# Optimization experiments

Hardware: AMD Instinct MI355X
Metric: run time of the kernel (lower is better)

## Reference

```python
import jax, jax.numpy as jnp
import numpy as np

B, L, IN_SZ, MEM_SZ = 32, 2048, 256, 256
W_SCALE = 0.05  # keep tanh/sigmoid out of saturation with random weights


def setup_inputs() -> dict:
    key = jax.random.key(0)
    ks = jax.random.split(key, 6)
    u = jax.random.normal(ks[0], (B, L, IN_SZ), dtype=jnp.float32)
    mk = lambda k, o, i: jax.random.normal(k, (o, i), dtype=jnp.float32) * W_SCALE
    return {
        "u": u,
        "W_ia": mk(ks[1], MEM_SZ, IN_SZ),
        "W_ha": mk(ks[2], MEM_SZ, MEM_SZ),
        "W_ic": mk(ks[3], MEM_SZ, IN_SZ),
        "W_hc": mk(ks[4], MEM_SZ, MEM_SZ),
        "W_io": mk(ks[5], MEM_SZ, IN_SZ),
    }


def reference(u, W_ia, W_ha, W_ic, W_hc, W_io):
    # u: [B, L, in_sz]; torch Linear: y = x @ W.T (no bias).
    b, l, _ = u.shape
    mem = W_ha.shape[0]
    # Precompute all input-side projections in 3 batched GEMMs (h-independent).
    xa = jnp.einsum('bli,mi->lbm', u, W_ia)  # [L,B,M]
    xc = jnp.einsum('bli,mi->lbm', u, W_ic)
    xo = jnp.einsum('bli,mi->lbm', u, W_io)

    def step(h, xs):
        xa_t, xc_t, xo_t = xs
        a = 1.0 + jnp.tanh(xa_t + h @ W_ha.T)
        c = jax.nn.sigmoid(xc_t + h @ W_hc.T)
        h_new = c * h + (1.0 - c) * jnp.tanh(xo_t + a * h)
        return h_new, h_new

    h0 = jnp.zeros((b, mem), dtype=u.dtype)
    _, hs = jax.lax.scan(step, h0, (xa, xc, xo))  # hs: [L,B,M]
    h_seq = jnp.transpose(hs, (1, 0, 2))  # [B,L,M]
    return h_seq, h_seq[:, -1:, :]
```

## Files before the change

### kernel.cpp

```cpp
#include <hip/hip_runtime.h>
#include <stdint.h>

#ifndef __has_builtin
#define __has_builtin(x) 0
#endif
#if __has_builtin(__builtin_amdgcn_fdot2)
#define HAVE_FDOT2 1
#else
#define HAVE_FDOT2 0
#endif

typedef float    f32x4 __attribute__((ext_vector_type(4)));
typedef _Float16 f16x2 __attribute__((ext_vector_type(2)));
typedef _Float16 f16x4 __attribute__((ext_vector_type(4)));
typedef _Float16 f16x8 __attribute__((ext_vector_type(8)));

#define NB 32
#define NL 2048
#define NM 256
#define NC 768
#define XS_SCALE 4096.0f
#define XS_INV   2.44140625e-4f

__device__ __forceinline__ float dot2f(f16x2 a, f16x2 b, float c) {
#if HAVE_FDOT2
  return __builtin_amdgcn_fdot2(a, b, c, false);
#else
  float d;
  asm("v_dot2_f32_f16 %0, %1, %2, %3" : "=v"(d) : "v"(a), "v"(b), "v"(c));
  return d;
#endif
}

__device__ __forceinline__ float tanh_fast(float x) {
  x = fminf(fmaxf(x, -30.f), 30.f);
  float e = __expf(-2.f * x);
  return (1.f - e) / (1.f + e);
}
__device__ __forceinline__ float sigmoid_fast(float x) {
  x = fminf(fmaxf(x, -30.f), 30.f);
  return 1.f / (1.f + __expf(-x));
}

__global__ __launch_bounds__(256) void proj_kernel(
    const float* __restrict__ u, const float* __restrict__ Wia,
    const float* __restrict__ Wic, const float* __restrict__ Wio,
    int16_t* __restrict__ xs)
{
  __shared__ _Float16 sAh[128][72];
  __shared__ _Float16 sAl[128][72];
  __shared__ _Float16 sBh[128][72];
  __shared__ _Float16 sBl[128][72];
  const int tid = threadIdx.x;
  const int rb = blockIdx.x, cb = blockIdx.y;
  const float* W = (cb < 2) ? Wia : (cb < 4) ? Wic : Wio;
  const int wrow0 = (cb & 1) * 128;

  const int wave = tid >> 6, lane = tid & 63;
  const int wr = (wave >> 1) * 64, wc = (wave & 1) * 64;
  const int lrow = lane & 15, lk = (lane >> 4) * 8;

  f32x4 acc[4][4] = {};

  for (int kt = 0; kt < 4; ++kt) {
#pragma unroll
    for (int i = 0; i < 8; ++i) {
      int idx = tid + 256 * i;
      int r = idx >> 4, c4 = idx & 15;
      f32x4 va = *reinterpret_cast<const f32x4*>(
          u + (size_t)(rb * 128 + r) * 256 + kt * 64 + c4 * 4);
      f16x4 hh, hl;
#pragma unroll
      for (int q = 0; q < 4; ++q) {
        _Float16 hi = (_Float16)va[q];
        hh[q] = hi;
        hl[q] = (_Float16)(va[q] - (float)hi);
      }
      *reinterpret_cast<f16x4*>(&sAh[r][c4 * 4]) = hh;
      *reinterpret_cast<f16x4*>(&sAl[r][c4 * 4]) = hl;
      f32x4 vb = *reinterpret_cast<const f32x4*>(
          W + (size_t)(wrow0 + r) * 256 + kt * 64 + c4 * 4);
      f16x4 gh, gl;
#pragma unroll
      for (int q = 0; q < 4; ++q) {
        _Float16 hi = (_Float16)vb[q];
        gh[q] = hi;
        gl[q] = (_Float16)(vb[q] - (float)hi);
      }
      *reinterpret_cast<f16x4*>(&sBh[r][c4 * 4]) = gh;
      *reinterpret_cast<f16x4*>(&sBl[r][c4 * 4]) = gl;
    }
    __syncthreads();
#pragma unroll
    for (int kk = 0; kk < 2; ++kk) {
      const int k0 = kk * 32 + lk;
      f16x8 afh[4], afl[4], bfh[4], bfl[4];
#pragma unroll
      for (int i = 0; i < 4; ++i) {
        afh[i] = *reinterpret_cast<const f16x8*>(&sAh[wr + i * 16 + lrow][k0]);
        afl[i] = *reinterpret_cast<const f16x8*>(&sAl[wr + i * 16 + lrow][k0]);
      }
#pragma unroll
      for (int j = 0; j < 4; ++j) {
        bfh[j] = *reinterpret_cast<const f16x8*>(&sBh[wc + j * 16 + lrow][k0]);
        bfl[j] = *reinterpret_cast<const f16x8*>(&sBl[wc + j * 16 + lrow][k0]);
      }
#pragma unroll
      for (int i = 0; i < 4; ++i)
#pragma unroll
        for (int j = 0; j < 4; ++j) {
          acc[i][j] = __builtin_amdgcn_mfma_f32_16x16x32_f16(afl[i], bfh[j], acc[i][j], 0, 0, 0);
          acc[i][j] = __builtin_amdgcn_mfma_f32_16x16x32_f16(afh[i], bfl[j], acc[i][j], 0, 0, 0);
          acc[i][j] = __builtin_amdgcn_mfma_f32_16x16x32_f16(afh[i], bfh[j], acc[i][j], 0, 0, 0);
        }
    }
    __syncthreads();
  }

  const size_t row0 = (size_t)rb * 128 + wr + (lane >> 4) * 4;
  const int col0 = cb * 128 + wc + (lane & 15);
#pragma unroll
  for (int i = 0; i < 4; ++i)
#pragma unroll
    for (int j = 0; j < 4; ++j)
#pragma unroll
      for (int q = 0; q < 4; ++q) {
        float v = acc[i][j][q] * XS_SCALE;
        v = fminf(fmaxf(v, -32767.f), 32767.f);
        xs[(row0 + i * 16 + q) * NC + (col0 + j * 16)] = (int16_t)__float2int_rn(v);
      }
}

__global__ __launch_bounds__(1024, 1) void rec_kernel(
    const float* __restrict__ Wha, const float* __restrict__ Whc,
    const int16_t* __restrict__ xs, float* __restrict__ out)
{
  __shared__ __align__(16) _Float16 hbuf[2][2][136];
  const int t = threadIdx.x;
  const int m = t >> 2;
  const int r = t & 3;
  const int g = r >> 1;
  const int ks = r & 1;
  const int b = blockIdx.x;

  const float* Wg = g ? Whc : Wha;
  f16x2 w[64];
#pragma unroll
  for (int j = 0; j < 32; ++j) {
    f32x4 v = *reinterpret_cast<const f32x4*>(Wg + (size_t)m * 256 + ks * 128 + j * 4);
    f16x2 p0; p0.x = (_Float16)v.x; p0.y = (_Float16)v.y;
    f16x2 p1; p1.x = (_Float16)v.z; p1.y = (_Float16)v.w;
    w[2 * j] = p0; w[2 * j + 1] = p1;
  }

  for (int idx = t; idx < 2 * 2 * 136; idx += 1024)
    reinterpret_cast<_Float16*>(hbuf)[idx] = (_Float16)0.f;
  __syncthreads();

  const int16_t* xrow = xs + (size_t)b * NL * NC;
  float* outb = out + (size_t)b * NL * NM;

  int pa0 = xrow[m],      pc0 = xrow[NM + m],      po0 = xrow[2 * NM + m];
  int pa1 = xrow[NC + m], pc1 = xrow[NC + NM + m], po1 = xrow[NC + 2 * NM + m];

  float h = 0.f;

#pragma unroll 2
  for (int l = 0; l < NL; ++l) {
    int na = 0, ncc = 0, no = 0;
    if (l + 2 < NL) {
      const int16_t* xr = xrow + (size_t)(l + 2) * NC;
      na = xr[m]; ncc = xr[NM + m]; no = xr[2 * NM + m];
    }

    const _Float16* hs = &hbuf[l & 1][ks][0];
    float a0 = 0.f, a1 = 0.f, a2 = 0.f, a3 = 0.f;
#pragma unroll
    for (int i = 0; i < 16; ++i) {
      f16x8 hv = *reinterpret_cast<const f16x8*>(hs + 8 * i);
      f16x2 h0; h0.x = hv[0]; h0.y = hv[1];
      f16x2 h1; h1.x = hv[2]; h1.y = hv[3];
      f16x2 h2; h2.x = hv[4]; h2.y = hv[5];
      f16x2 h3; h3.x = hv[6]; h3.y = hv[7];
      a0 = dot2f(h0, w[4 * i + 0], a0);
      a1 = dot2f(h1, w[4 * i + 1], a1);
      a2 = dot2f(h2, w[4 * i + 2], a2);
      a3 = dot2f(h3, w[4 * i + 3], a3);
    }
    float acc = (a0 + a1) + (a2 + a3);
    acc += __shfl_xor(acc, 1);
    float other = __shfl_xor(acc, 2);
    float sa = g ? other : acc;
    float sc = g ? acc : other;

    float xa = (float)pa0 * XS_INV;
    float xc = (float)pc0 * XS_INV;
    float xo = (float)po0 * XS_INV;
    float a = 1.f + tanh_fast(xa + sa);
    float c = sigmoid_fast(xc + sc);
    float hn = c * h + (1.f - c) * tanh_fast(xo + a * h);
    h = hn;
    if (r == 0) {
      outb[(size_t)l * NM + m] = hn;
      hbuf[(l + 1) & 1][m >> 7][m & 127] = (_Float16)hn;
    }
    pa0 = pa1; pc0 = pc1; po0 = po1;
    pa1 = na;  pc1 = ncc; po1 = no;
    __syncthreads();
  }
  if (r == 0) out[(size_t)NB * NL * NM + (size_t)b * NM + m] = h;
}

extern "C" void kernel_launch(void* const* d_in, const int* in_sizes, int n_in,
                              void* d_out, int out_size, void* d_ws, size_t ws_size,
                              hipStream_t stream) {
  (void)in_sizes; (void)n_in; (void)out_size; (void)ws_size;
  const float* u   = (const float*)d_in[0];
  const float* Wia = (const float*)d_in[1];
  const float* Wha = (const float*)d_in[2];
  const float* Wic = (const float*)d_in[3];
  const float* Whc = (const float*)d_in[4];
  const float* Wio = (const float*)d_in[5];
  float* out = (float*)d_out;
  int16_t* xs = (int16_t*)d_ws;

  proj_kernel<<<dim3(512, 6), 256, 0, stream>>>(u, Wia, Wic, Wio, xs);
  rec_kernel<<<NB, 1024, 0, stream>>>(Wha, Whc, xs, out);
}
```

Baseline: 2.864 ms.

## Stream pre-converted fp16 recurrent weights from global memory instead of registers

Adds a small kernel that converts W_ha/W_hc to fp16 in a coalesced per-wave layout. The recurrent kernel then reloads these weights from L1/L2 on every timestep instead of holding 64 packed registers per thread. Launch bounds are changed to allow more waves per SIMD, and the cross-lane reductions use ds_swizzle instead of shfl. The aim is to cut register pressure and shuffle cost, at the price of 128 KB of weight reads per block on every one of 2048 serial steps.

```diff
diff --git a/kernel.cpp b/kernel.cpp
--- a/kernel.cpp
+++ b/kernel.cpp
@@ -14,6 +14,7 @@
 typedef _Float16 f16x2 __attribute__((ext_vector_type(2)));
 typedef _Float16 f16x4 __attribute__((ext_vector_type(4)));
 typedef _Float16 f16x8 __attribute__((ext_vector_type(8)));
+typedef uint32_t u32x4 __attribute__((ext_vector_type(4)));
 
 #define NB 32
 #define NL 2048
@@ -21,6 +22,7 @@
 #define NC 768
 #define XS_SCALE 4096.0f
 #define XS_INV   2.44140625e-4f
+#define XS_BYTES ((size_t)65536 * 768 * 2)
 
 __device__ __forceinline__ float dot2f(f16x2 a, f16x2 b, float c) {
 #if HAVE_FDOT2
@@ -32,6 +34,16 @@
 #endif
 }
 
+__device__ __forceinline__ float dot2u(uint32_t hbits, uint32_t wbits, float c) {
+  return dot2f(__builtin_bit_cast(f16x2, hbits), __builtin_bit_cast(f16x2, wbits), c);
+}
+
+template <int PAT>
+__device__ __forceinline__ float swz(float v) {
+  int r = __builtin_amdgcn_ds_swizzle(__builtin_bit_cast(int, v), PAT);
+  return __builtin_bit_cast(float, r);
+}
+
 __device__ __forceinline__ float tanh_fast(float x) {
   x = fminf(fmaxf(x, -30.f), 30.f);
   float e = __expf(-2.f * x);
@@ -40,6 +52,23 @@
 __device__ __forceinline__ float sigmoid_fast(float x) {
   x = fminf(fmaxf(x, -30.f), 30.f);
   return 1.f / (1.f + __expf(-x));
+}
+
+__global__ __launch_bounds__(256) void wconv_kernel(
+    const float* __restrict__ Wha, const float* __restrict__ Whc,
+    _Float16* __restrict__ wf16)
+{
+  int cidx = blockIdx.x * 256 + threadIdx.x;
+  int w = cidx >> 10, rem = cidx & 1023;
+  int j = rem >> 6, l = rem & 63;
+  int t = w * 64 + l;
+  int m = t >> 2, r = t & 3;
+  int g = r >> 1, ks = r & 1;
+  const float* src = (g ? Whc : Wha) + (size_t)m * 256 + ks * 128 + j * 8;
+  f16x8 o;
+#pragma unroll
+  for (int e = 0; e < 8; ++e) o[e] = (_Float16)src[e];
+  *reinterpret_cast<f16x8*>(wf16 + (size_t)cidx * 8) = o;
 }
 
 __global__ __launch_bounds__(256) void proj_kernel(
@@ -131,8 +160,8 @@
       }
 }
 
-__global__ __launch_bounds__(1024, 1) void rec_kernel(
-    const float* __restrict__ Wha, const float* __restrict__ Whc,
+__global__ __launch_bounds__(1024, 4) void rec_kernel(
+    const _Float16* __restrict__ wf16,
     const int16_t* __restrict__ xs, float* __restrict__ out)
 {
   __shared__ __align__(16) _Float16 hbuf[2][2][136];
@@ -140,18 +169,13 @@
   const int m = t >> 2;
   const int r = t & 3;
   const int g = r >> 1;
-  const int ks = r & 1;
   const int b = blockIdx.x;
 
-  const float* Wg = g ? Whc : Wha;
-  f16x2 w[64];
-#pragma unroll
-  for (int j = 0; j < 32; ++j) {
-    f32x4 v = *reinterpret_cast<const f32x4*>(Wg + (size_t)m * 256 + ks * 128 + j * 4);
-    f16x2 p0; p0.x = (_Float16)v.x; p0.y = (_Float16)v.y;
-    f16x2 p1; p1.x = (_Float16)v.z; p1.y = (_Float16)v.w;
-    w[2 * j] = p0; w[2 * j + 1] = p1;
-  }
+  const char* wp = (const char*)wf16 + (size_t)(t >> 6) * 16384 + (size_t)(t & 63) * 16;
+  const char* wq0 = wp;
+  const char* wq1 = wp + 4096;
+  const char* wq2 = wp + 8192;
+  const char* wq3 = wp + 12288;
 
   for (int idx = t; idx < 2 * 2 * 136; idx += 1024)
     reinterpret_cast<_Float16*>(hbuf)[idx] = (_Float16)0.f;
@@ -173,23 +197,25 @@
       na = xr[m]; ncc = xr[NM + m]; no = xr[2 * NM + m];
     }
 
-    const _Float16* hs = &hbuf[l & 1][ks][0];
+    const u32x4* hs = reinterpret_cast<const u32x4*>(&hbuf[l & 1][r & 1][0]);
     float a0 = 0.f, a1 = 0.f, a2 = 0.f, a3 = 0.f;
 #pragma unroll
-    for (int i = 0; i < 16; ++i) {
-      f16x8 hv = *reinterpret_cast<const f16x8*>(hs + 8 * i);
-      f16x2 h0; h0.x = hv[0]; h0.y = hv[1];
-      f16x2 h1; h1.x = hv[2]; h1.y = hv[3];
-      f16x2 h2; h2.x = hv[4]; h2.y = hv[5];
-      f16x2 h3; h3.x = hv[6]; h3.y = hv[7];
-      a0 = dot2f(h0, w[4 * i + 0], a0);
-      a1 = dot2f(h1, w[4 * i + 1], a1);
-      a2 = dot2f(h2, w[4 * i + 2], a2);
-      a3 = dot2f(h3, w[4 * i + 3], a3);
+    for (int q = 0; q < 4; ++q) {
+      const char* wq = (q == 0) ? wq0 : (q == 1) ? wq1 : (q == 2) ? wq2 : wq3;
+#pragma unroll
+      for (int jj = 0; jj < 4; ++jj) {
+        const int j = q * 4 + jj;
+        u32x4 wv = *reinterpret_cast<const u32x4*>(wq + jj * 1024);
+        u32x4 hv = hs[j];
+        a0 = dot2u(hv.x, wv.x, a0);
+        a1 = dot2u(hv.y, wv.y, a1);
+        a2 = dot2u(hv.z, wv.z, a2);
+        a3 = dot2u(hv.w, wv.w, a3);
+      }
     }
     float acc = (a0 + a1) + (a2 + a3);
-    acc += __shfl_xor(acc, 1);
-    float other = __shfl_xor(acc, 2);
+    acc += swz<0x041F>(acc);
+    float other = swz<0x081F>(acc);
     float sa = g ? other : acc;
     float sc = g ? acc : other;
 
@@ -223,7 +249,9 @@
   const float* Wio = (const float*)d_in[5];
   float* out = (float*)d_out;
   int16_t* xs = (int16_t*)d_ws;
-
+  _Float16* wf16 = (_Float16*)((char*)d_ws + XS_BYTES);
+
+  wconv_kernel<<<64, 256, 0, stream>>>(Wha, Whc, wf16);
   proj_kernel<<<dim3(512, 6), 256, 0, stream>>>(u, Wia, Wic, Wio, xs);
-  rec_kernel<<<NB, 1024, 0, stream>>>(Wha, Whc, xs, out);
-}
+  rec_kernel<<<NB, 1024, 0, stream>>>(wf16, xs, out);
+}
```

After: 2.843 ms. Within noise of the previous version (-0.7%).
